# Optimization experiments

Measured on AMD Instinct MI355X. Metric: run time of the kernel, lower is better.

## Reference

```python
import jax, jax.numpy as jnp
import numpy as np
from jax import lax

B, C, H, W = 16, 128, 64, 64
AUX = 2 * 128 + 20 + 1  # hybrid: edge(128)+seg(128)+pred_edge(1)+pred_seg(20)
PATCHES = [(2, 2), (4, 4)]


def conv1x1(x, w, b):
    # w: [O, I]
    return jnp.einsum('bchw,oc->bohw', x, w) + b[None, :, None, None]


def conv3x3(x, w, b, pad, dil=1):
    y = lax.conv_general_dilated(x, w, (1, 1), [(pad, pad), (pad, pad)],
                                 rhs_dilation=(dil, dil),
                                 dimension_numbers=('NCHW', 'OIHW', 'NCHW'))
    return y + b[None, :, None, None]


def layernorm_chw(x, eps=1e-5):
    # LayerNorm over [C,H,W] per sample, no affine
    mu = x.mean(axis=(1, 2, 3), keepdims=True)
    var = ((x - mu) ** 2).mean(axis=(1, 2, 3), keepdims=True)
    return (x - mu) / jnp.sqrt(var + eps)


def adn(x, aux, ew, eb, sw, sb, bw, bb):
    a = conv1x1(aux, ew, eb)
    gamma = conv1x1(a, sw, sb)
    beta = conv1x1(jnp.concatenate([x, a], axis=1), bw, bb)
    return layernorm_chw(x) * gamma + beta


def window_attn(q, k, v, ph, pw):
    b, dk, h, w = q.shape
    oh, ow = h // ph, w // pw

    def patch(t):  # [b,dk,h,w] -> [b, oh*ow, dk*ph*pw]
        t = t.reshape(b, dk, oh, ph, ow, pw)
        return t.transpose(0, 2, 4, 1, 3, 5).reshape(b, oh * ow, dk * ph * pw)

    Q, K, V = patch(q), patch(k), patch(v)
    scale = 1.0 / jnp.sqrt(jnp.asarray(Q.shape[-1], Q.dtype))
    scores = jnp.einsum('bnd,bmd->bnm', Q, K) * scale
    y = jnp.einsum('bnm,bmd->bnd', jax.nn.softmax(scores, axis=-1), V)
    y = y.reshape(b, oh, ow, dk, ph, pw).transpose(0, 3, 1, 4, 2, 5).reshape(b, dk, h, w)
    return y


def mssa_forward(p):
    (x, edge, seg, pred_edge, pred_seg,
     q_w, q_b, k_w, k_b, v_w, v_b,
     d1_embed_w, d1_embed_b, d1_scale_w, d1_scale_b, d1_bias_w, d1_bias_b,
     d2_embed_w, d2_embed_b, d2_scale_w, d2_scale_b, d2_bias_w, d2_bias_b,
     sc_w, sc_b, bi1_w, bi1_b, bi2_w, bi2_b) = p

    aux = jnp.concatenate([edge, seg, pred_edge, pred_seg], axis=1)

    q = adn(conv1x1(x, q_w, q_b), aux, d1_embed_w, d1_embed_b, d1_scale_w, d1_scale_b, d1_bias_w, d1_bias_b)
    k = adn(conv1x1(x, k_w, k_b), aux, d1_embed_w, d1_embed_b, d1_scale_w, d1_scale_b, d1_bias_w, d1_bias_b)
    v = adn(conv1x1(x, v_w, v_b), aux, d1_embed_w, d1_embed_b, d1_scale_w, d1_scale_b, d1_bias_w, d1_bias_b)

    qs = jnp.split(q, len(PATCHES), axis=1)
    ks = jnp.split(k, len(PATCHES), axis=1)
    vs = jnp.split(v, len(PATCHES), axis=1)
    outs = [window_attn(qs[i], ks[i], vs[i], PATCHES[i][1], PATCHES[i][0]) for i in range(len(PATCHES))]

    mid = x + jnp.concatenate(outs, axis=1)
    o = adn(mid, aux, d2_embed_w, d2_embed_b, d2_scale_w, d2_scale_b, d2_bias_w, d2_bias_b)
    gamma = jnp.tanh(conv3x3(o, sc_w, sc_b, pad=1))
    beta = conv3x3(jax.nn.gelu(conv3x3(o, bi1_w, bi1_b, pad=2, dil=2), approximate=False), bi2_w, bi2_b, pad=1)
    return mid * gamma + beta


def setup_inputs() -> dict:
    key = jax.random.key(0)
    ks = iter(jax.random.split(key, 40))
    nrm = lambda shape, s=1.0: jax.random.normal(next(ks), shape, jnp.float32) * s
    P = 0.02  # param init scale
    inp = {
        'x': nrm((B, C, H, W)),
        'edge': nrm((B, 128, H, W)),
        'seg': nrm((B, 128, H, W)),
        'pred_edge': jax.random.uniform(next(ks), (B, 1, H, W), jnp.float32),
        'pred_seg': jax.random.uniform(next(ks), (B, 20, H, W), jnp.float32),
        'q_w': nrm((C, C), P), 'q_b': jnp.zeros((C,), jnp.float32),
        'k_w': nrm((C, C), P), 'k_b': jnp.zeros((C,), jnp.float32),
        'v_w': nrm((C, C), P), 'v_b': jnp.zeros((C,), jnp.float32),
        'd1_embed_w': nrm((C, AUX), P), 'd1_embed_b': jnp.zeros((C,), jnp.float32),
        'd1_scale_w': nrm((C, C), P), 'd1_scale_b': jnp.ones((C,), jnp.float32),
        'd1_bias_w': nrm((C, 2 * C), P), 'd1_bias_b': jnp.zeros((C,), jnp.float32),
        'd2_embed_w': nrm((C, AUX), P), 'd2_embed_b': jnp.zeros((C,), jnp.float32),
        'd2_scale_w': nrm((C, C), P), 'd2_scale_b': jnp.ones((C,), jnp.float32),
        'd2_bias_w': nrm((C, 2 * C), P), 'd2_bias_b': jnp.zeros((C,), jnp.float32),
        'sc_w': nrm((C, C, 3, 3), P), 'sc_b': jnp.zeros((C,), jnp.float32),
        'bi1_w': nrm((C, C, 3, 3), P), 'bi1_b': jnp.zeros((C,), jnp.float32),
        'bi2_w': nrm((C, C, 3, 3), P), 'bi2_b': jnp.zeros((C,), jnp.float32),
    }
    return inp


def reference(x, edge, seg, pred_edge, pred_seg,
              q_w, q_b, k_w, k_b, v_w, v_b,
              d1_embed_w, d1_embed_b, d1_scale_w, d1_scale_b, d1_bias_w, d1_bias_b,
              d2_embed_w, d2_embed_b, d2_scale_w, d2_scale_b, d2_bias_w, d2_bias_b,
              sc_w, sc_b, bi1_w, bi1_b, bi2_w, bi2_b):
    return mssa_forward((x, edge, seg, pred_edge, pred_seg,
                         q_w, q_b, k_w, k_b, v_w, v_b,
                         d1_embed_w, d1_embed_b, d1_scale_w, d1_scale_b, d1_bias_w, d1_bias_b,
                         d2_embed_w, d2_embed_b, d2_scale_w, d2_scale_b, d2_bias_w, d2_bias_b,
                         sc_w, sc_b, bi1_w, bi1_b, bi2_w, bi2_b))
```

## Files before the change

### kernel.cpp

```cpp
#include <hip/hip_runtime.h>
#include <cstdint>

typedef unsigned short ushort_t;
typedef unsigned int uint_t;
typedef __attribute__((ext_vector_type(8))) short short8;
typedef __attribute__((ext_vector_type(4))) float f32x4;

#define MFMA16(a, b, c) __builtin_amdgcn_mfma_f32_16x16x32_bf16((a), (b), (c), 0, 0, 0)
#define SWZ(c, r) ((((c) + ((r) >> 2)) & 3))
#define INV_N 1.9073486328125e-6f

struct P4 { ushort_t* p[4]; };
struct B4 { const float* b[4]; };

__device__ __forceinline__ ushort_t f2bf(float f) {
    uint_t u = __builtin_bit_cast(uint_t, f);
    u += 0x7FFFu + ((u >> 16) & 1u);
    return (ushort_t)(u >> 16);
}
__device__ __forceinline__ float bf2f(ushort_t h) {
    return __builtin_bit_cast(float, (uint_t)h << 16);
}

__global__ __launch_bounds__(256) void prep_w(
    ushort_t* wb, const float* qw, const float* kw, const float* vw,
    const float* ew1, const float* ew2, const float* sw1, const float* sw2,
    const float* bw1, const float* bw2,
    const float* scw, const float* b1w, const float* b2w)
{
    int idx = blockIdx.x * 256 + threadIdx.x;
    if (idx >= 663552) return;
    float v;
    if (idx < 49152) {
        int z = idx >> 14, r = idx & 16383;
        v = (z == 0 ? qw : z == 1 ? kw : vw)[r];
    } else if (idx < 122880) {
        int j = idx - 49152; int z = j / 36864; int jj = j - z * 36864;
        int o = jj / 288, k = jj - o * 288;
        v = (k < 277) ? (z ? ew2 : ew1)[o * 277 + k] : 0.f;
    } else if (idx < 155648) {
        int j = idx - 122880; int z = j >> 14;
        v = (z ? sw2 : sw1)[j & 16383];
    } else if (idx < 221184) {
        int j = idx - 155648; int z = j >> 15;
        v = (z ? bw2 : bw1)[j & 32767];
    } else {
        int j = idx - 221184;
        const float* src = j < 147456 ? scw : j < 294912 ? b1w : b2w;
        j = j % 147456;
        int tap = j >> 14, r = (j >> 7) & 127, c = j & 127;
        v = src[r * 1152 + c * 9 + tap];
    }
    wb[idx] = f2bf(v);
}

__global__ __launch_bounds__(256) void combine_w(ushort_t* wc, const ushort_t* wb)
{
    __shared__ float ews[128 * 33];
    __shared__ ushort_t Ws[128 * 130];
    int z = blockIdx.y, nt = blockIdx.x, n0 = nt * 32;
    int t = threadIdx.x;
    const ushort_t* wew = wb + 49152;
    const ushort_t* wsw = wb + 122880;
    const ushort_t* wbw = wb + 155648;
    const ushort_t* W; int wstr, wof;
    if (z == 0)      { W = wsw;         wstr = 128; wof = 0; }
    else if (z == 1) { W = wbw;         wstr = 256; wof = 128; }
    else if (z == 2) { W = wsw + 16384; wstr = 128; wof = 0; }
    else             { W = wbw + 32768; wstr = 256; wof = 128; }
    const ushort_t* E = wew + (z >= 2 ? 36864 : 0);
    for (int s = t; s < 16384; s += 256) {
        int c = s & 127, o = s >> 7;
        Ws[c * 130 + o] = W[o * wstr + wof + c];
    }
    for (int s = t; s < 4096; s += 256) {
        int c = s >> 5, n = s & 31;
        ews[c * 33 + n] = bf2f(E[c * 288 + n0 + n]);
    }
    __syncthreads();
    int o = t & 127, nh = t >> 7;
    float acc[16];
#pragma unroll
    for (int i = 0; i < 16; ++i) acc[i] = 0.f;
    for (int c = 0; c < 128; ++c) {
        float wv = bf2f(Ws[c * 130 + o]);
#pragma unroll
        for (int i = 0; i < 16; ++i) acc[i] += wv * ews[c * 33 + nh * 16 + i];
    }
#pragma unroll
    for (int i = 0; i < 16; ++i)
        wc[(size_t)(z * 128 + o) * 288 + n0 + nh * 16 + i] = f2bf(acc[i]);
}

__global__ __launch_bounds__(512) void combine_bias(
    float* bc, const float* sw1, const float* bw1, const float* sw2, const float* bw2,
    const float* eb1, const float* eb2, const float* sb1, const float* bb1,
    const float* sb2, const float* bb2)
{
    int t = threadIdx.x; int z = t >> 7, o = t & 127;
    const float* W; int wstr, wof; const float* eb; float add;
    if (z == 0)      { W = sw1; wstr = 128; wof = 0;   eb = eb1; add = sb1[o]; }
    else if (z == 1) { W = bw1; wstr = 256; wof = 128; eb = eb1; add = bb1[o]; }
    else if (z == 2) { W = sw2; wstr = 128; wof = 0;   eb = eb2; add = sb2[o]; }
    else             { W = bw2; wstr = 256; wof = 128; eb = eb2; add = bb2[o]; }
    float s = add;
    for (int c = 0; c < 128; ++c) s += W[o * wstr + wof + c] * eb[c];
    bc[t] = s;
}

__global__ __launch_bounds__(256) void transp_x(const float* __restrict__ x, ushort_t* __restrict__ xT)
{
    __shared__ ushort_t tile[64 * 130];
    int b = blockIdx.y, p0 = blockIdx.x * 64;
    int t = threadIdx.x;
#pragma unroll
    for (int i = 0; i < 8; ++i) {
        int s = t + i * 256;
        int c = s >> 4, p4 = (s & 15) * 4;
        float4 f = *(const float4*)(x + ((size_t)(b * 128 + c) << 12) + p0 + p4);
        tile[(p4 + 0) * 130 + c] = f2bf(f.x);
        tile[(p4 + 1) * 130 + c] = f2bf(f.y);
        tile[(p4 + 2) * 130 + c] = f2bf(f.z);
        tile[(p4 + 3) * 130 + c] = f2bf(f.w);
    }
    __syncthreads();
#pragma unroll
    for (int i = 0; i < 4; ++i) {
        int s = t + i * 256;
        int p = s >> 4, c8 = (s & 15) * 8;
        ushort_t v[8];
#pragma unroll
        for (int e = 0; e < 8; ++e) v[e] = tile[p * 130 + c8 + e];
        uint4 ov = {(uint_t)v[0] | ((uint_t)v[1] << 16), (uint_t)v[2] | ((uint_t)v[3] << 16),
                    (uint_t)v[4] | ((uint_t)v[5] << 16), (uint_t)v[6] | ((uint_t)v[7] << 16)};
        *(uint4*)(xT + ((size_t)(b * 4096) + p0 + p) * 128 + c8) = ov;
    }
}

__global__ __launch_bounds__(256) void transp_aux(const float* __restrict__ edge, const float* __restrict__ seg,
                                                  const float* __restrict__ pe, const float* __restrict__ ps,
                                                  ushort_t* __restrict__ auxT)
{
    __shared__ ushort_t tile[64 * 292];
    int b = blockIdx.y, p0 = blockIdx.x * 64;
    int t = threadIdx.x;
#pragma unroll
    for (int i = 0; i < 18; ++i) {
        int s = t + i * 256;
        int c = s >> 4, p4 = (s & 15) * 4;
        float4 f = {0.f, 0.f, 0.f, 0.f};
        if (c < 128)       f = *(const float4*)(edge + ((size_t)(b * 128 + c) << 12) + p0 + p4);
        else if (c < 256)  f = *(const float4*)(seg + ((size_t)(b * 128 + c - 128) << 12) + p0 + p4);
        else if (c == 256) f = *(const float4*)(pe + ((size_t)b << 12) + p0 + p4);
        else if (c < 277)  f = *(const float4*)(ps + ((size_t)(b * 20 + c - 257) << 12) + p0 + p4);
        tile[(p4 + 0) * 292 + c] = f2bf(f.x);
        tile[(p4 + 1) * 292 + c] = f2bf(f.y);
        tile[(p4 + 2) * 292 + c] = f2bf(f.z);
        tile[(p4 + 3) * 292 + c] = f2bf(f.w);
    }
    __syncthreads();
#pragma unroll
    for (int i = 0; i < 9; ++i) {
        int s = t + i * 256;
        int p = s / 36, c8 = (s % 36) * 8;
        ushort_t v[8];
#pragma unroll
        for (int e = 0; e < 8; ++e) v[e] = tile[p * 292 + c8 + e];
        uint4 ov = {(uint_t)v[0] | ((uint_t)v[1] << 16), (uint_t)v[2] | ((uint_t)v[3] << 16),
                    (uint_t)v[4] | ((uint_t)v[5] << 16), (uint_t)v[6] | ((uint_t)v[7] << 16)};
        *(uint4*)(auxT + ((size_t)(b * 4096) + p0 + p) * 288 + c8) = ov;
    }
}

template <int EP>
__global__ __launch_bounds__(256) void gemm_conv(
    const ushort_t* bA, int Kb1, size_t zBoff,
    const ushort_t* wA, int wstride, int wAperZ, int NK,
    B4 bias4, P4 out4, const ushort_t* gT, const ushort_t* betT,
    float* stats, int dostats)
{
    constexpr int LDSZ = (EP == 2) ? 33792 : 34816;
    __shared__ char lds[LDSZ];
    int b = blockIdx.y, bx = blockIdx.x, z = blockIdx.z;
    int t = threadIdx.x, lane = t & 63, w = t >> 6;
    int wm = w & 1, wn = w >> 1, lo = lane & 15, quad = lane >> 4;
    const ushort_t* wAz = wA + (wAperZ ? (size_t)z * 128 * wstride : 0);
    const ushort_t* bAz = bA + (size_t)z * zBoff;
    ushort_t* outp = out4.p[z];
    size_t bbase = (size_t)b * 4096;
    int y0 = 0, x0 = 0;
    if (EP == 2) { y0 = (bx >> 1) * 4; x0 = (bx & 1) * 32; }

    f32x4 acc[4][4];
#pragma unroll
    for (int i = 0; i < 4; ++i)
#pragma unroll
        for (int j = 0; j < 4; ++j) acc[i][j] = (f32x4){0.f, 0.f, 0.f, 0.f};

    int r0 = t >> 2, c0 = t & 3, r1 = r0 + 64;
    int gp0, gp1;
    if (EP == 2) {
        gp0 = (y0 + (r0 >> 5)) * 64 + x0 + (r0 & 31);
        gp1 = (y0 + (r1 >> 5)) * 64 + x0 + (r1 & 31);
    } else {
        gp0 = bx * 128 + r0;
        gp1 = bx * 128 + r1;
    }
    const ushort_t* bRow0 = bAz + (bbase + gp0) * Kb1;
    const ushort_t* bRow1 = bAz + (bbase + gp1) * Kb1;
    uint4 pfA0 = *(const uint4*)(wAz + (size_t)r0 * wstride + c0 * 8);
    uint4 pfA1 = *(const uint4*)(wAz + (size_t)r1 * wstride + c0 * 8);
    uint4 pfB0 = *(const uint4*)(bRow0 + c0 * 8);
    uint4 pfB1 = *(const uint4*)(bRow1 + c0 * 8);
    for (int ck = 0; ck < NK; ++ck) {
        __syncthreads();
        *(uint4*)(lds + r0 * 64 + SWZ(c0, r0) * 16) = pfA0;
        *(uint4*)(lds + r1 * 64 + SWZ(c0, r1) * 16) = pfA1;
        *(uint4*)(lds + 8192 + r0 * 64 + SWZ(c0, r0) * 16) = pfB0;
        *(uint4*)(lds + 8192 + r1 * 64 + SWZ(c0, r1) * 16) = pfB1;
        __syncthreads();
        if (ck + 1 < NK) {
            int k0 = (ck + 1) * 32;
            pfA0 = *(const uint4*)(wAz + (size_t)r0 * wstride + k0 + c0 * 8);
            pfA1 = *(const uint4*)(wAz + (size_t)r1 * wstride + k0 + c0 * 8);
            pfB0 = *(const uint4*)(bRow0 + k0 + c0 * 8);
            pfB1 = *(const uint4*)(bRow1 + k0 + c0 * 8);
        }
        short8 af[4];
#pragma unroll
        for (int mt = 0; mt < 4; ++mt) {
            int row = wm * 64 + mt * 16 + lo;
            af[mt] = *(const short8*)(lds + row * 64 + SWZ(quad, row) * 16);
        }
#pragma unroll
        for (int nt = 0; nt < 4; ++nt) {
            int n = wn * 64 + nt * 16 + lo;
            short8 bf = *(const short8*)(lds + 8192 + n * 64 + SWZ(quad, n) * 16);
#pragma unroll
            for (int mt = 0; mt < 4; ++mt) acc[mt][nt] = MFMA16(af[mt], bf, acc[mt][nt]);
        }
    }

    float mean = 0.f, rstd = 0.f;
    if (EP >= 2) {
        int slot = (EP == 3) ? 3 : z;
        float s0 = stats[(slot * 16 + b) * 2], s1 = stats[(slot * 16 + b) * 2 + 1];
        mean = s0 * INV_N;
        rstd = rsqrtf(fmaxf(s1 * INV_N - mean * mean, 0.f) + 1e-5f);
    }
    float lsum = 0.f, lss = 0.f;
    if (EP == 2) {
        __syncthreads();
        ushort_t* Cs = (ushort_t*)lds;
#pragma unroll
        for (int mt = 0; mt < 4; ++mt)
#pragma unroll
            for (int nt = 0; nt < 4; ++nt) {
                int oo0 = wm * 64 + mt * 16 + quad * 4;
                int pp = wn * 64 + nt * 16 + lo;
                int gp = (y0 + (pp >> 5)) * 64 + x0 + (pp & 31);
                size_t tbase = (bbase + gp) * 128 + oo0;
                ushort4 tv = *(const ushort4*)(bAz + tbase);
                ushort4 gv = *(const ushort4*)(gT + tbase);
                ushort4 bv = *(const ushort4*)(betT + tbase);
#pragma unroll
                for (int r = 0; r < 4; ++r) {
                    float v = acc[mt][nt][r] + bf2f((&bv.x)[r])
                            + (bf2f((&tv.x)[r]) - mean) * rstd * bf2f((&gv.x)[r]);
                    Cs[(oo0 + r) * 132 + pp] = f2bf(v);
                }
            }
        __syncthreads();
        if (z < 2) {
            for (int s = t; s < 1024; s += 256) {
                int n_l = s >> 5, fq = s & 31;
                int ypair = n_l >> 4, xp = n_l & 15;
                ushort_t tmp[8];
#pragma unroll
                for (int e = 0; e < 8; ++e) {
                    int f = fq * 8 + e;
                    int c = f >> 2, py = (f >> 1) & 1, px = f & 1;
                    tmp[e] = Cs[c * 132 + (ypair * 2 + py) * 32 + xp * 2 + px];
                }
                int n = ((y0 >> 1) + ypair) * 32 + (x0 >> 1) + xp;
                uint4 ov = {(uint_t)tmp[0] | ((uint_t)tmp[1] << 16), (uint_t)tmp[2] | ((uint_t)tmp[3] << 16),
                            (uint_t)tmp[4] | ((uint_t)tmp[5] << 16), (uint_t)tmp[6] | ((uint_t)tmp[7] << 16)};
                *(uint4*)(outp + ((size_t)(b * 1024 + n) << 8) + fq * 8) = ov;
            }
            for (int s = t; s < 1024; s += 256) {
                int n_l = s >> 7, fq = s & 127;
                ushort_t tmp[8];
#pragma unroll
                for (int e = 0; e < 8; ++e) {
                    int f = fq * 8 + e;
                    int c = f >> 4, py = (f >> 2) & 3, px = f & 3;
                    tmp[e] = Cs[(64 + c) * 132 + py * 32 + n_l * 4 + px];
                }
                int n = (y0 >> 2) * 16 + (x0 >> 2) + n_l;
                uint4 ov = {(uint_t)tmp[0] | ((uint_t)tmp[1] << 16), (uint_t)tmp[2] | ((uint_t)tmp[3] << 16),
                            (uint_t)tmp[4] | ((uint_t)tmp[5] << 16), (uint_t)tmp[6] | ((uint_t)tmp[7] << 16)};
                *(uint4*)(outp + 4194304u + ((size_t)(b * 256 + n) << 10) + fq * 8) = ov;
            }
        } else {
            for (int s = t; s < 2048; s += 256) {
                int f = s >> 3, j = s & 7;
                int ypair = j >> 2, xq = j & 3;
                int c = f >> 2, py = (f >> 1) & 1, px = f & 1;
                ushort_t tmp[4];
#pragma unroll
                for (int i2 = 0; i2 < 4; ++i2)
                    tmp[i2] = Cs[c * 132 + (ypair * 2 + py) * 32 + (xq * 4 + i2) * 2 + px];
                int m0 = ((y0 >> 1) + ypair) * 32 + (x0 >> 1) + xq * 4;
                uint2 ov = {(uint_t)tmp[0] | ((uint_t)tmp[1] << 16), (uint_t)tmp[2] | ((uint_t)tmp[3] << 16)};
                *(uint2*)(outp + ((size_t)(b * 256 + f) << 10) + m0) = ov;
            }
            for (int s = t; s < 2048; s += 256) {
                int f = s >> 1, j = s & 1;
                int c = f >> 4, py = (f >> 2) & 3, px = f & 3;
                ushort_t tmp[4];
#pragma unroll
                for (int i2 = 0; i2 < 4; ++i2)
                    tmp[i2] = Cs[(64 + c) * 132 + py * 32 + (j * 4 + i2) * 4 + px];
                int m0 = (y0 >> 2) * 16 + (x0 >> 2) + j * 4;
                uint2 ov = {(uint_t)tmp[0] | ((uint_t)tmp[1] << 16), (uint_t)tmp[2] | ((uint_t)tmp[3] << 16)};
                *(uint2*)(outp + 4194304u + ((size_t)(b * 1024 + f) << 8) + m0) = ov;
            }
        }
    } else {
        ushort_t* Cs = (ushort_t*)lds;
        __syncthreads();
#pragma unroll
        for (int mt = 0; mt < 4; ++mt)
#pragma unroll
            for (int nt = 0; nt < 4; ++nt) {
                int oo0 = wm * 64 + mt * 16 + quad * 4;
                int pp = wn * 64 + nt * 16 + lo;
                float vv[4];
                if (EP == 0) {
#pragma unroll
                    for (int r = 0; r < 4; ++r) vv[r] = acc[mt][nt][r] + bias4.b[z][oo0 + r];
                    if (dostats) {
#pragma unroll
                        for (int r = 0; r < 4; ++r) { lsum += vv[r]; lss += vv[r] * vv[r]; }
                    }
                } else {
                    size_t tbase = (bbase + bx * 128 + pp) * 128 + oo0;
                    ushort4 tv = *(const ushort4*)(bAz + tbase);
                    ushort4 gv = *(const ushort4*)(gT + tbase);
                    ushort4 bv = *(const ushort4*)(betT + tbase);
#pragma unroll
                    for (int r = 0; r < 4; ++r)
                        vv[r] = acc[mt][nt][r] + bf2f((&bv.x)[r])
                              + (bf2f((&tv.x)[r]) - mean) * rstd * bf2f((&gv.x)[r]);
                }
                ushort4 st = {f2bf(vv[0]), f2bf(vv[1]), f2bf(vv[2]), f2bf(vv[3])};
                *(ushort4*)(&Cs[pp * 136 + oo0]) = st;
            }
        __syncthreads();
        if (EP == 3) {
#pragma unroll
            for (int i = 0; i < 2; ++i) {
                int c = t + i * 256;
                int cc2 = c >> 7, pp = c & 127;
                size_t dst = ((size_t)(b * 4 + cc2) * 4096 + bx * 128 + pp) * 32;
#pragma unroll
                for (int j = 0; j < 4; ++j)
                    *(uint4*)(outp + dst + j * 8) = *(const uint4*)(&Cs[pp * 136 + cc2 * 32 + j * 8]);
            }
        } else {
            int pp = t >> 1, hf = t & 1;
            size_t gofs = (bbase + bx * 128 + pp) * 128 + hf * 64;
#pragma unroll
            for (int i = 0; i < 8; ++i)
                *(uint4*)(outp + gofs + i * 8) = *(const uint4*)(&Cs[pp * 136 + hf * 64 + i * 8]);
        }
    }
    if (EP == 0 && dostats) {
#pragma unroll
        for (int o2 = 32; o2 >= 1; o2 >>= 1) { lsum += __shfl_xor(lsum, o2); lss += __shfl_xor(lss, o2); }
        __syncthreads();
        float* red = (float*)lds;
        if (lane == 0) { red[w * 2] = lsum; red[w * 2 + 1] = lss; }
        __syncthreads();
        if (t == 0) {
            atomicAdd(&stats[(z * 16 + b) * 2], red[0] + red[2] + red[4] + red[6]);
            atomicAdd(&stats[(z * 16 + b) * 2 + 1], red[1] + red[3] + red[5] + red[7]);
        }
    }
}

template <int EP>
__global__ __launch_bounds__(256) void gemm_attn(
    const ushort_t* A, size_t aBS, const ushort_t* Bm, size_t bBS,
    int Ka, int NK, float scale,
    ushort_t* sout, size_t soBS, int soNb,
    const ushort_t* xT, ushort_t* midT, float* stats)
{
    constexpr int LDSZ = (EP >= 1) ? 33792 : 34816;
    __shared__ char lds[LDSZ];
    int b = blockIdx.z, my = blockIdx.y, nx = blockIdx.x;
    int t = threadIdx.x, lane = t & 63, w = t >> 6;
    int wm = w & 1, wn = w >> 1, lo = lane & 15, quad = lane >> 4;

    f32x4 acc[4][4];
#pragma unroll
    for (int i = 0; i < 4; ++i)
#pragma unroll
        for (int j = 0; j < 4; ++j) acc[i][j] = (f32x4){0.f, 0.f, 0.f, 0.f};

    const ushort_t* Ab = A + b * aBS + (size_t)(my * 128) * Ka;
    const ushort_t* Bb = Bm + b * bBS + (size_t)(nx * 128) * Ka;
    int r0 = t >> 2, c0 = t & 3, r1 = r0 + 64;
    uint4 pfA0 = *(const uint4*)(Ab + (size_t)r0 * Ka + c0 * 8);
    uint4 pfA1 = *(const uint4*)(Ab + (size_t)r1 * Ka + c0 * 8);
    uint4 pfB0 = *(const uint4*)(Bb + (size_t)r0 * Ka + c0 * 8);
    uint4 pfB1 = *(const uint4*)(Bb + (size_t)r1 * Ka + c0 * 8);
    for (int ck = 0; ck < NK; ++ck) {
        __syncthreads();
        *(uint4*)(lds + r0 * 64 + SWZ(c0, r0) * 16) = pfA0;
        *(uint4*)(lds + r1 * 64 + SWZ(c0, r1) * 16) = pfA1;
        *(uint4*)(lds + 8192 + r0 * 64 + SWZ(c0, r0) * 16) = pfB0;
        *(uint4*)(lds + 8192 + r1 * 64 + SWZ(c0, r1) * 16) = pfB1;
        __syncthreads();
        if (ck + 1 < NK) {
            int k0 = (ck + 1) * 32;
            pfA0 = *(const uint4*)(Ab + (size_t)r0 * Ka + k0 + c0 * 8);
            pfA1 = *(const uint4*)(Ab + (size_t)r1 * Ka + k0 + c0 * 8);
            pfB0 = *(const uint4*)(Bb + (size_t)r0 * Ka + k0 + c0 * 8);
            pfB1 = *(const uint4*)(Bb + (size_t)r1 * Ka + k0 + c0 * 8);
        }
        short8 af[4];
#pragma unroll
        for (int mt = 0; mt < 4; ++mt) {
            int row = wm * 64 + mt * 16 + lo;
            af[mt] = *(const short8*)(lds + row * 64 + SWZ(quad, row) * 16);
        }
#pragma unroll
        for (int nt = 0; nt < 4; ++nt) {
            int n = wn * 64 + nt * 16 + lo;
            short8 bf = *(const short8*)(lds + 8192 + n * 64 + SWZ(quad, n) * 16);
#pragma unroll
            for (int mt = 0; mt < 4; ++mt) acc[mt][nt] = MFMA16(af[mt], bf, acc[mt][nt]);
        }
    }

    if (EP == 0) {
        ushort_t* Cs = (ushort_t*)lds;
        __syncthreads();
#pragma unroll
        for (int mt = 0; mt < 4; ++mt)
#pragma unroll
            for (int nt = 0; nt < 4; ++nt) {
                int rr0 = wm * 64 + mt * 16 + quad * 4;
                int cl = wn * 64 + nt * 16 + lo;
                ushort4 st = {f2bf(acc[mt][nt][0] * scale), f2bf(acc[mt][nt][1] * scale),
                              f2bf(acc[mt][nt][2] * scale), f2bf(acc[mt][nt][3] * scale)};
                *(ushort4*)(&Cs[cl * 136 + rr0]) = st;
            }
        __syncthreads();
        {
            int rr = t >> 1, hf = t & 1;
            size_t gbase = (size_t)b * soBS + (size_t)(my * 128 + rr) * soNb + nx * 128 + hf * 64;
#pragma unroll
            for (int i = 0; i < 8; ++i) {
                ushort_t e[8];
#pragma unroll
                for (int j = 0; j < 8; ++j) e[j] = Cs[(hf * 64 + i * 8 + j) * 136 + rr];
                uint4 ov = {(uint_t)e[0] | ((uint_t)e[1] << 16), (uint_t)e[2] | ((uint_t)e[3] << 16),
                            (uint_t)e[4] | ((uint_t)e[5] << 16), (uint_t)e[6] | ((uint_t)e[7] << 16)};
                *(uint4*)(sout + gbase + i * 8) = ov;
            }
        }
        return;
    }
    __syncthreads();
    ushort_t* Cs = (ushort_t*)lds;
#pragma unroll
    for (int mt = 0; mt < 4; ++mt)
#pragma unroll
        for (int nt = 0; nt < 4; ++nt)
#pragma unroll
            for (int reg = 0; reg < 4; ++reg) {
                int r_l = wm * 64 + mt * 16 + quad * 4 + reg;
                int c_l = wn * 64 + nt * 16 + lo;
                Cs[r_l * 132 + c_l] = f2bf(acc[mt][nt][reg]);
            }
    __syncthreads();
    float lsum = 0.f, lss = 0.f;
    for (int s = t; s < 4096; s += 256) {
        int sp, r_l, cbase, pybit, pxbit;
        if (EP == 1) {
            int sp_l = s >> 3, cj = s & 7;
            int y_l = sp_l >> 6, xv = sp_l & 63;
            r_l = (y_l >> 1) * 32 + (xv >> 1);
            sp = (my * 8 + y_l) * 64 + xv;
            cbase = nx * 32 + cj * 4;
            pybit = (y_l & 1) * 2 + (xv & 1);
            pxbit = 4;
        } else {
            int sp_l = s >> 1, cj = s & 1;
            int y_l = sp_l >> 6, xv = sp_l & 63;
            r_l = (y_l >> 2) * 16 + (xv >> 2);
            sp = (my * 32 + y_l) * 64 + xv;
            cbase = 64 + nx * 8 + cj * 4;
            pybit = (y_l & 3) * 4 + (xv & 3);
            pxbit = 16;
        }
        size_t base = ((size_t)(b * 4096) + sp) * 128 + cbase;
        ushort4 xv4 = *(const ushort4*)(xT + base);
        int c_l0 = (EP == 1) ? (cbase - nx * 32) * 4 + pybit : (cbase - 64 - nx * 8) * 16 + pybit;
        ushort_t o4[4];
#pragma unroll
        for (int ci = 0; ci < 4; ++ci) {
            float vm = bf2f(Cs[r_l * 132 + c_l0 + ci * pxbit]) + bf2f((&xv4.x)[ci]);
            o4[ci] = f2bf(vm);
            lsum += vm; lss += vm * vm;
        }
        ushort4 st = {o4[0], o4[1], o4[2], o4[3]};
        *(ushort4*)(midT + base) = st;
    }
#pragma unroll
    for (int o2 = 32; o2 >= 1; o2 >>= 1) { lsum += __shfl_xor(lsum, o2); lss += __shfl_xor(lss, o2); }
    __syncthreads();
    float* red = (float*)lds;
    if (lane == 0) { red[w * 2] = lsum; red[w * 2 + 1] = lss; }
    __syncthreads();
    if (t == 0) {
        atomicAdd(&stats[(3 * 16 + b) * 2], red[0] + red[2] + red[4] + red[6]);
        atomicAdd(&stats[(3 * 16 + b) * 2 + 1], red[1] + red[3] + red[5] + red[7]);
    }
}

__global__ __launch_bounds__(256) void softmax_k(ushort_t* SP)
{
    int wid = blockIdx.x * 4 + (threadIdx.x >> 6);
    int lane = threadIdx.x & 63;
    ushort_t* row;
    int PL;
    if (wid < 16384) { row = SP + ((size_t)wid << 10); PL = 16; }
    else { int r2 = wid - 16384; row = SP + 16777216u + ((size_t)r2 << 8); PL = 4; }
    float v[16];
    float mx = -1e30f;
    for (int i = 0; i < PL; ++i) { v[i] = bf2f(row[lane + (i << 6)]); mx = fmaxf(mx, v[i]); }
#pragma unroll
    for (int o = 32; o >= 1; o >>= 1) mx = fmaxf(mx, __shfl_xor(mx, o));
    float sum = 0.f;
    for (int i = 0; i < PL; ++i) { v[i] = __expf(v[i] - mx); sum += v[i]; }
#pragma unroll
    for (int o = 32; o >= 1; o >>= 1) sum += __shfl_xor(sum, o);
    float inv = 1.f / sum;
    for (int i = 0; i < PL; ++i) row[lane + (i << 6)] = f2bf(v[i] * inv);
}

__global__ __launch_bounds__(1024) void conv3x3_dual(
    const ushort_t* __restrict__ inT, const ushort_t* __restrict__ wtA, const ushort_t* __restrict__ wtB,
    const float* __restrict__ biasA, const float* __restrict__ biasB,
    ushort_t* __restrict__ outA, ushort_t* __restrict__ outB)
{
    __shared__ char lds[73728 + 12 * 68 * 64];
    char* Braw = lds + 73728;
    int b = blockIdx.y, z = blockIdx.z;
    int dil = 1 + z;
    int NRr = 8 + 2 * dil;
    const ushort_t* wt = z ? wtB : wtA;
    const float* bias = z ? biasB : biasA;
    ushort_t* out = z ? outB : outA;
    int y0 = blockIdx.x * 8;
    int t = threadIdx.x, lane = t & 63, w = t >> 6;
    int wm = w & 1, wr = w >> 1, lo = lane & 15, quad = lane >> 4;

    f32x4 acc[4][4];
#pragma unroll
    for (int i = 0; i < 4; ++i)
#pragma unroll
        for (int j = 0; j < 4; ++j) acc[i][j] = (f32x4){0.f, 0.f, 0.f, 0.f};

    for (int cc = 0; cc < 4; ++cc) {
        if (cc) __syncthreads();
        for (int s = t; s < 4608; s += 1024) {
            int tap = s >> 9, r = (s >> 2) & 127, c = s & 3;
            uint4 v = *(const uint4*)(wt + ((size_t)(tap * 128 + r) << 7) + cc * 32 + c * 8);
            *(uint4*)(lds + tap * 8192 + r * 64 + SWZ(c, r) * 16) = v;
        }
        int NSLOT = NRr * 272;
        for (int s = t; s < NSLOT; s += 1024) {
            int c4 = s & 3;
            int pr = s >> 2;
            int xx = pr % 68, rr = pr / 68;
            int ys = y0 - dil + rr;
            int ix = xx - dil;
            uint4 v = {0u, 0u, 0u, 0u};
            if (ys >= 0 && ys < 64 && (unsigned)ix < 64u)
                v = *(const uint4*)(inT + ((size_t)((b * 4 + cc) * 4096 + ys * 64 + ix)) * 32 + c4 * 8);
            *(uint4*)(Braw + pr * 64 + SWZ(c4, pr) * 16) = v;
        }
        __syncthreads();
#pragma unroll
        for (int tap = 0; tap < 9; ++tap) {
            int ky = tap / 3, kx = tap % 3;
            short8 af[4];
#pragma unroll
            for (int mt = 0; mt < 4; ++mt) {
                int row = wm * 64 + mt * 16 + lo;
                af[mt] = *(const short8*)(lds + tap * 8192 + row * 64 + SWZ(quad, row) * 16);
            }
#pragma unroll
            for (int nt = 0; nt < 4; ++nt) {
                int pr = (wr + ky * dil) * 68 + nt * 16 + lo + kx * dil;
                short8 bf = *(const short8*)(Braw + pr * 64 + SWZ(quad, pr) * 16);
#pragma unroll
                for (int mt = 0; mt < 4; ++mt) acc[mt][nt] = MFMA16(af[mt], bf, acc[mt][nt]);
            }
        }
    }
    for (int h = 0; h < 2; ++h) {
        __syncthreads();
        if ((wr >> 2) == h) {
            int rl = wr & 3;
#pragma unroll
            for (int mt = 0; mt < 4; ++mt)
#pragma unroll
                for (int nt = 0; nt < 4; ++nt) {
                    int oo0 = wm * 64 + mt * 16 + quad * 4;
                    int col = nt * 16 + lo;
                    ushort4 st;
#pragma unroll
                    for (int r = 0; r < 4; ++r) {
                        float v = acc[mt][nt][r] + bias[oo0 + r];
                        if (z == 0) v = tanhf(v);
                        else        v = 0.5f * v * (1.f + erff(v * 0.70710678118654752f));
                        (&st.x)[r] = f2bf(v);
                    }
                    int byo = ((rl * 64 + col) * 256 + oo0 * 2) ^ ((col & 15) << 4);
                    *(ushort4*)(lds + byo) = st;
                }
        }
        __syncthreads();
        if (z == 0) {
            int rl2 = t >> 8, col2 = (t >> 2) & 63, k2 = t & 3;
            char* dst = (char*)out + (((size_t)(b * 4096) + (y0 + h * 4 + rl2) * 64 + col2) << 8) + k2 * 64;
            int bb = (rl2 * 64 + col2) * 256 + k2 * 64;
            int sw = (col2 & 15) << 4;
#pragma unroll
            for (int i = 0; i < 4; ++i)
                *(uint4*)(dst + i * 16) = *(const uint4*)(lds + ((bb + i * 16) ^ sw));
        } else {
            int cc2 = t >> 8, s_l = t & 255;
            int rl2 = s_l >> 6, col2 = s_l & 63;
            ushort_t* dst = out + ((size_t)((b * 4 + cc2) * 4096) + (y0 + h * 4 + rl2) * 64 + col2) * 32;
            int bb = (rl2 * 64 + col2) * 256 + cc2 * 64;
            int sw = (col2 & 15) << 4;
#pragma unroll
            for (int i = 0; i < 4; ++i)
                *(uint4*)(dst + i * 8) = *(const uint4*)(lds + ((bb + i * 16) ^ sw));
        }
    }
}

__global__ __launch_bounds__(512) void conv3x3_final(
    const ushort_t* __restrict__ inT, const ushort_t* __restrict__ wt, const float* __restrict__ bias,
    float* __restrict__ out, const ushort_t* __restrict__ midT, const ushort_t* __restrict__ g3T)
{
    __shared__ char lds[73728 + 6 * 68 * 64];
    char* Braw = lds + 73728;
    int b = blockIdx.y;
    int y0 = blockIdx.x * 4;
    int t = threadIdx.x, lane = t & 63, w = t >> 6;
    int wm = w & 1, wr = w >> 1, lo = lane & 15, quad = lane >> 4;

    f32x4 acc[4][4];
#pragma unroll
    for (int i = 0; i < 4; ++i)
#pragma unroll
        for (int j = 0; j < 4; ++j) acc[i][j] = (f32x4){0.f, 0.f, 0.f, 0.f};

    for (int cc = 0; cc < 4; ++cc) {
        if (cc) __syncthreads();
        for (int s = t; s < 4608; s += 512) {
            int tap = s >> 9, r = (s >> 2) & 127, c = s & 3;
            uint4 v = *(const uint4*)(wt + ((size_t)(tap * 128 + r) << 7) + cc * 32 + c * 8);
            *(uint4*)(lds + tap * 8192 + r * 64 + SWZ(c, r) * 16) = v;
        }
        for (int s = t; s < 1632; s += 512) {
            int c4 = s & 3;
            int pr = s >> 2;
            int xx = pr % 68, rr = pr / 68;
            int ys = y0 - 1 + rr;
            int ix = xx - 1;
            uint4 v = {0u, 0u, 0u, 0u};
            if (ys >= 0 && ys < 64 && (unsigned)ix < 64u)
                v = *(const uint4*)(inT + ((size_t)((b * 4 + cc) * 4096 + ys * 64 + ix)) * 32 + c4 * 8);
            *(uint4*)(Braw + pr * 64 + SWZ(c4, pr) * 16) = v;
        }
        __syncthreads();
#pragma unroll
        for (int tap = 0; tap < 9; ++tap) {
            int ky = tap / 3, kx = tap % 3;
            short8 af[4];
#pragma unroll
            for (int mt = 0; mt < 4; ++mt) {
                int row = wm * 64 + mt * 16 + lo;
                af[mt] = *(const short8*)(lds + tap * 8192 + row * 64 + SWZ(quad, row) * 16);
            }
#pragma unroll
            for (int nt = 0; nt < 4; ++nt) {
                int pr = (wr + ky) * 68 + nt * 16 + lo + kx;
                short8 bf = *(const short8*)(Braw + pr * 64 + SWZ(quad, pr) * 16);
#pragma unroll
                for (int mt = 0; mt < 4; ++mt) acc[mt][nt] = MFMA16(af[mt], bf, acc[mt][nt]);
            }
        }
    }
#pragma unroll
    for (int mt = 0; mt < 4; ++mt)
#pragma unroll
        for (int nt = 0; nt < 4; ++nt) {
            int oo0 = wm * 64 + mt * 16 + quad * 4;
            int col = nt * 16 + lo;
            int sp = (y0 + wr) * 64 + col;
            size_t tbase = ((size_t)(b * 4096) + sp) * 128 + oo0;
            ushort4 mv = *(const ushort4*)(midT + tbase);
            ushort4 gv = *(const ushort4*)(g3T + tbase);
#pragma unroll
            for (int r = 0; r < 4; ++r) {
                int oo = oo0 + r;
                size_t off = ((size_t)(b * 128 + oo) << 12) + sp;
                out[off] = bf2f((&mv.x)[r]) * bf2f((&gv.x)[r]) + acc[mt][nt][r] + bias[oo];
            }
        }
}

extern "C" void kernel_launch(void* const* d_in, const int* in_sizes, int n_in,
                              void* d_out, int out_size, void* d_ws, size_t ws_size,
                              hipStream_t stream)
{
    const float* x    = (const float*)d_in[0];
    const float* edge = (const float*)d_in[1];
    const float* seg  = (const float*)d_in[2];
    const float* pe   = (const float*)d_in[3];
    const float* ps   = (const float*)d_in[4];
    const float* q_w  = (const float*)d_in[5];  const float* q_b  = (const float*)d_in[6];
    const float* k_w  = (const float*)d_in[7];  const float* k_b  = (const float*)d_in[8];
    const float* v_w  = (const float*)d_in[9];  const float* v_b  = (const float*)d_in[10];
    const float* d1_ew = (const float*)d_in[11]; const float* d1_eb = (const float*)d_in[12];
    const float* d1_sw = (const float*)d_in[13]; const float* d1_sb = (const float*)d_in[14];
    const float* d1_bw = (const float*)d_in[15]; const float* d1_bb = (const float*)d_in[16];
    const float* d2_ew = (const float*)d_in[17]; const float* d2_eb = (const float*)d_in[18];
    const float* d2_sw = (const float*)d_in[19]; const float* d2_sb = (const float*)d_in[20];
    const float* d2_bw = (const float*)d_in[21]; const float* d2_bb = (const float*)d_in[22];
    const float* sc_w  = (const float*)d_in[23]; const float* sc_b  = (const float*)d_in[24];
    const float* bi1_w = (const float*)d_in[25]; const float* bi1_b = (const float*)d_in[26];
    const float* bi2_w = (const float*)d_in[27]; const float* bi2_b = (const float*)d_in[28];

    char* ws = (char*)d_ws;
    ushort_t* wb = (ushort_t*)ws;
    ushort_t* wc = (ushort_t*)(ws + 1327360);
    float* bc    = (float*)(ws + 1622272);
    float* stats = (float*)(ws + 1624320);
    char* RA = ws + 1703936;
    char* RB = RA + 37748736;
    char* RC = RB + 16777216;
    char* RD = RC + 50331648;
    char* RE = RD + 16777216;
    char* RF = RE + 16777216;
    char* RG = RF + 16777216;
    char* RH = RG + 16777216;
    char* RI = RH + 33554432;

    ushort_t* auxT = (ushort_t*)RA;
    ushort_t* SP0  = (ushort_t*)RA;
    ushort_t* xT   = (ushort_t*)RB;
    ushort_t* q0T  = (ushort_t*)RC;
    ushort_t* midT = (ushort_t*)RC;
    ushort_t* oT   = (ushort_t*)(RC + 16777216);
    ushort_t* g1   = (ushort_t*)RD;
    ushort_t* g3   = (ushort_t*)RD;
    ushort_t* betA1= (ushort_t*)RE;
    ushort_t* g2   = (ushort_t*)RF;
    ushort_t* betA2= (ushort_t*)RG;
    ushort_t* Qp   = (ushort_t*)RH;
    ushort_t* Kp   = Qp + 8388608;
    ushort_t* VT   = (ushort_t*)RI;
    ushort_t* tT   = (ushort_t*)RI;
    const size_t ZB = 8388608;

    dim3 blk(256);

    hipMemsetAsync(stats, 0, 512, stream);
    prep_w<<<2592, blk, 0, stream>>>(wb, q_w, k_w, v_w, d1_ew, d2_ew, d1_sw, d2_sw, d1_bw, d2_bw, sc_w, bi1_w, bi2_w);
    combine_bias<<<1, 512, 0, stream>>>(bc, d1_sw, d1_bw, d2_sw, d2_bw, d1_eb, d2_eb, d1_sb, d1_bb, d2_sb, d2_bb);
    combine_w<<<dim3(9, 4), blk, 0, stream>>>(wc, wb);
    transp_x<<<dim3(64, 16), blk, 0, stream>>>(x, xT);
    transp_aux<<<dim3(64, 16), blk, 0, stream>>>(edge, seg, pe, ps, auxT);

    gemm_conv<0><<<dim3(32, 16, 4), blk, 0, stream>>>(auxT, 288, 0, wc, 288, 1, 9,
        B4{{bc, bc + 128, bc + 256, bc + 384}}, P4{{g1, betA1, g2, betA2}}, nullptr, nullptr, stats, 0);
    gemm_conv<0><<<dim3(32, 16, 3), blk, 0, stream>>>(xT, 128, 0, wb, 128, 1, 4,
        B4{{q_b, k_b, v_b, nullptr}}, P4{{q0T, q0T + ZB, q0T + 2 * ZB, nullptr}}, nullptr, nullptr, stats, 1);
    gemm_conv<2><<<dim3(32, 16, 3), blk, 0, stream>>>(q0T, 128, ZB, wb + 155648, 256, 0, 4,
        B4{{nullptr, nullptr, nullptr, nullptr}}, P4{{Qp, Kp, VT, nullptr}}, g1, betA1, stats, 0);

    gemm_attn<0><<<dim3(8, 8, 16), blk, 0, stream>>>(Qp, 262144, Kp, 262144, 256, 8, 0.0625f,
        SP0, 1048576, 1024, nullptr, nullptr, stats);
    gemm_attn<0><<<dim3(2, 2, 16), blk, 0, stream>>>(Qp + 4194304, 262144, Kp + 4194304, 262144, 1024, 32, 0.03125f,
        SP0 + 16777216, 65536, 256, nullptr, nullptr, stats);
    softmax_k<<<5120, blk, 0, stream>>>(SP0);
    gemm_attn<1><<<dim3(2, 8, 16), blk, 0, stream>>>(SP0, 1048576, VT, 262144, 1024, 32, 1.f,
        nullptr, 0, 0, xT, midT, stats);
    gemm_attn<2><<<dim3(8, 2, 16), blk, 0, stream>>>(SP0 + 16777216, 65536, VT + 4194304, 262144, 256, 8, 1.f,
        nullptr, 0, 0, xT, midT, stats);

    gemm_conv<3><<<dim3(32, 16, 1), blk, 0, stream>>>(midT, 128, 0, wb + 155648 + 32768, 256, 0, 4,
        B4{{nullptr, nullptr, nullptr, nullptr}}, P4{{oT, nullptr, nullptr, nullptr}}, g2, betA2, stats, 0);

    conv3x3_dual<<<dim3(8, 16, 2), dim3(1024), 0, stream>>>(oT, wb + 221184, wb + 368640, sc_b, bi1_b, g3, tT);
    conv3x3_final<<<dim3(16, 16), dim3(512), 0, stream>>>(tT, wb + 516096, bi2_b, (float*)d_out, midT, g3);
}
```

Measured before the change: 649.4 us.

## Stack multiple output-weight slabs per block to reuse activation tiles

Measured after the change: 735.1 us. +13.2%, slower.

```diff
diff --git a/kernel.cpp b/kernel.cpp
--- a/kernel.cpp
+++ b/kernel.cpp
@@ -172,6 +172,117 @@
     }
 }
 
+template <int NS, int DOSTATS>
+__global__ __launch_bounds__(NS * 256) void gemm_stack(
+    const ushort_t* __restrict__ bA, int K, const ushort_t* __restrict__ Wstk, int NK,
+    B4 bias4, P4 out4, float* stats)
+{
+    constexpr int STAGE = NS * 8192 + 8192;
+    constexpr int LDSZ = (STAGE > 34816) ? STAGE : 34816;
+    __shared__ char lds[LDSZ];
+    int b = blockIdx.y, bx = blockIdx.x;
+    int t = threadIdx.x, lane = t & 63, w = t >> 6;
+    int wm = w >> 1, wn = w & 1, lo = lane & 15, quad = lane >> 4;
+    size_t bbase = (size_t)b * 4096;
+
+    f32x4 acc[4][4];
+#pragma unroll
+    for (int i = 0; i < 4; ++i)
+#pragma unroll
+        for (int j = 0; j < 4; ++j) acc[i][j] = (f32x4){0.f, 0.f, 0.f, 0.f};
+
+    const int TOT = (NS + 1) * 512;
+    uint4 pf[3];
+#pragma unroll
+    for (int i = 0; i < 3; ++i) {
+        int s = t + i * NS * 256;
+        if (s < TOT) {
+            if (s < NS * 512) { int q = s >> 2, c = s & 3; pf[i] = *(const uint4*)(Wstk + (size_t)q * K + c * 8); }
+            else { int r = (s - NS * 512) >> 2, c = s & 3; pf[i] = *(const uint4*)(bA + (bbase + bx * 128 + r) * (size_t)K + c * 8); }
+        }
+    }
+    for (int ck = 0; ck < NK; ++ck) {
+        __syncthreads();
+#pragma unroll
+        for (int i = 0; i < 3; ++i) {
+            int s = t + i * NS * 256;
+            if (s < TOT) {
+                int off;
+                if (s < NS * 512) { int q = s >> 2, c = s & 3; off = q * 64 + SWZ(c, q) * 16; }
+                else { int r = (s - NS * 512) >> 2, c = s & 3; off = NS * 8192 + r * 64 + SWZ(c, r) * 16; }
+                *(uint4*)(lds + off) = pf[i];
+            }
+        }
+        __syncthreads();
+        if (ck + 1 < NK) {
+            int k0 = (ck + 1) * 32;
+#pragma unroll
+            for (int i = 0; i < 3; ++i) {
+                int s = t + i * NS * 256;
+                if (s < TOT) {
+                    if (s < NS * 512) { int q = s >> 2, c = s & 3; pf[i] = *(const uint4*)(Wstk + (size_t)q * K + k0 + c * 8); }
+                    else { int r = (s - NS * 512) >> 2, c = s & 3; pf[i] = *(const uint4*)(bA + (bbase + bx * 128 + r) * (size_t)K + k0 + c * 8); }
+                }
+            }
+        }
+        short8 af[4];
+#pragma unroll
+        for (int mt = 0; mt < 4; ++mt) {
+            int row = wm * 64 + mt * 16 + lo;
+            af[mt] = *(const short8*)(lds + row * 64 + SWZ(quad, row) * 16);
+        }
+#pragma unroll
+        for (int nt = 0; nt < 4; ++nt) {
+            int n = wn * 64 + nt * 16 + lo;
+            short8 bf = *(const short8*)(lds + NS * 8192 + n * 64 + SWZ(quad, n) * 16);
+#pragma unroll
+            for (int mt = 0; mt < 4; ++mt) acc[mt][nt] = MFMA16(af[mt], bf, acc[mt][nt]);
+        }
+    }
+
+    ushort_t* Cs = (ushort_t*)lds;
+    for (int z = 0; z < NS; ++z) {
+        __syncthreads();
+        if ((wm >> 1) == z) {
+            float lsum = 0.f, lss = 0.f;
+#pragma unroll
+            for (int mt = 0; mt < 4; ++mt)
+#pragma unroll
+                for (int nt = 0; nt < 4; ++nt) {
+                    int oo0 = (wm & 1) * 64 + mt * 16 + quad * 4;
+                    int pp = wn * 64 + nt * 16 + lo;
+                    float vv[4];
+#pragma unroll
+                    for (int r = 0; r < 4; ++r) vv[r] = acc[mt][nt][r] + bias4.b[z][oo0 + r];
+                    if (DOSTATS) {
+#pragma unroll
+                        for (int r = 0; r < 4; ++r) { lsum += vv[r]; lss += vv[r] * vv[r]; }
+                    }
+                    ushort4 st = {f2bf(vv[0]), f2bf(vv[1]), f2bf(vv[2]), f2bf(vv[3])};
+                    *(ushort4*)(&Cs[pp * 136 + oo0]) = st;
+                }
+            if (DOSTATS) {
+#pragma unroll
+                for (int o2 = 32; o2 >= 1; o2 >>= 1) { lsum += __shfl_xor(lsum, o2); lss += __shfl_xor(lss, o2); }
+                if (lane == 0) {
+                    atomicAdd(&stats[(z * 16 + b) * 2], lsum);
+                    atomicAdd(&stats[(z * 16 + b) * 2 + 1], lss);
+                }
+            }
+        }
+        __syncthreads();
+        ushort_t* outp = out4.p[z];
+#pragma unroll
+        for (int i = 0; i < 3; ++i) {
+            int c3 = t + i * NS * 256;
+            if (c3 < 2048) {
+                int pp = c3 >> 4, ii = c3 & 15;
+                *(uint4*)(outp + (bbase + bx * 128 + pp) * 128 + ii * 8) = *(const uint4*)(&Cs[pp * 136 + ii * 8]);
+            }
+        }
+    }
+}
+
 template <int EP>
 __global__ __launch_bounds__(256) void gemm_conv(
     const ushort_t* bA, int Kb1, size_t zBoff,
@@ -242,13 +353,12 @@
     }
 
     float mean = 0.f, rstd = 0.f;
-    if (EP >= 2) {
+    {
         int slot = (EP == 3) ? 3 : z;
         float s0 = stats[(slot * 16 + b) * 2], s1 = stats[(slot * 16 + b) * 2 + 1];
         mean = s0 * INV_N;
         rstd = rsqrtf(fmaxf(s1 * INV_N - mean * mean, 0.f) + 1e-5f);
     }
-    float lsum = 0.f, lss = 0.f;
     if (EP == 2) {
         __syncthreads();
         ushort_t* Cs = (ushort_t*)lds;
@@ -336,55 +446,26 @@
                 int oo0 = wm * 64 + mt * 16 + quad * 4;
                 int pp = wn * 64 + nt * 16 + lo;
                 float vv[4];
-                if (EP == 0) {
-#pragma unroll
-                    for (int r = 0; r < 4; ++r) vv[r] = acc[mt][nt][r] + bias4.b[z][oo0 + r];
-                    if (dostats) {
-#pragma unroll
-                        for (int r = 0; r < 4; ++r) { lsum += vv[r]; lss += vv[r] * vv[r]; }
-                    }
-                } else {
-                    size_t tbase = (bbase + bx * 128 + pp) * 128 + oo0;
-                    ushort4 tv = *(const ushort4*)(bAz + tbase);
-                    ushort4 gv = *(const ushort4*)(gT + tbase);
-                    ushort4 bv = *(const ushort4*)(betT + tbase);
-#pragma unroll
-                    for (int r = 0; r < 4; ++r)
-                        vv[r] = acc[mt][nt][r] + bf2f((&bv.x)[r])
-                              + (bf2f((&tv.x)[r]) - mean) * rstd * bf2f((&gv.x)[r]);
-                }
+                size_t tbase = (bbase + bx * 128 + pp) * 128 + oo0;
+                ushort4 tv = *(const ushort4*)(bAz + tbase);
+                ushort4 gv = *(const ushort4*)(gT + tbase);
+                ushort4 bv = *(const ushort4*)(betT + tbase);
+#pragma unroll
+                for (int r = 0; r < 4; ++r)
+                    vv[r] = acc[mt][nt][r] + bf2f((&bv.x)[r])
+                          + (bf2f((&tv.x)[r]) - mean) * rstd * bf2f((&gv.x)[r]);
                 ushort4 st = {f2bf(vv[0]), f2bf(vv[1]), f2bf(vv[2]), f2bf(vv[3])};
                 *(ushort4*)(&Cs[pp * 136 + oo0]) = st;
             }
         __syncthreads();
-        if (EP == 3) {
-#pragma unroll
-            for (int i = 0; i < 2; ++i) {
-                int c = t + i * 256;
-                int cc2 = c >> 7, pp = c & 127;
-                size_t dst = ((size_t)(b * 4 + cc2) * 4096 + bx * 128 + pp) * 32;
-#pragma unroll
-                for (int j = 0; j < 4; ++j)
-                    *(uint4*)(outp + dst + j * 8) = *(const uint4*)(&Cs[pp * 136 + cc2 * 32 + j * 8]);
-            }
-        } else {
-            int pp = t >> 1, hf = t & 1;
-            size_t gofs = (bbase + bx * 128 + pp) * 128 + hf * 64;
-#pragma unroll
-            for (int i = 0; i < 8; ++i)
-                *(uint4*)(outp + gofs + i * 8) = *(const uint4*)(&Cs[pp * 136 + hf * 64 + i * 8]);
-        }
-    }
-    if (EP == 0 && dostats) {
-#pragma unroll
-        for (int o2 = 32; o2 >= 1; o2 >>= 1) { lsum += __shfl_xor(lsum, o2); lss += __shfl_xor(lss, o2); }
-        __syncthreads();
-        float* red = (float*)lds;
-        if (lane == 0) { red[w * 2] = lsum; red[w * 2 + 1] = lss; }
-        __syncthreads();
-        if (t == 0) {
-            atomicAdd(&stats[(z * 16 + b) * 2], red[0] + red[2] + red[4] + red[6]);
-            atomicAdd(&stats[(z * 16 + b) * 2 + 1], red[1] + red[3] + red[5] + red[7]);
+#pragma unroll
+        for (int i = 0; i < 2; ++i) {
+            int c = t + i * 256;
+            int cc2 = c >> 7, pp = c & 127;
+            size_t dst = ((size_t)(b * 4 + cc2) * 4096 + bx * 128 + pp) * 32;
+#pragma unroll
+            for (int j = 0; j < 4; ++j)
+                *(uint4*)(outp + dst + j * 8) = *(const uint4*)(&Cs[pp * 136 + cc2 * 32 + j * 8]);
         }
     }
 }
@@ -678,7 +759,7 @@
         if (cc) __syncthreads();
         for (int s = t; s < 4608; s += 512) {
             int tap = s >> 9, r = (s >> 2) & 127, c = s & 3;
-            uint4 v = *(const uint4*)(wt + ((size_t)(tap * 128 + r) << 7) + cc * 32 + c * 8);
+            uint4 v = *(const uint4*)(wt + ((size_t)((tap)*128 + r) << 7) + cc * 32 + c * 8);
             *(uint4*)(lds + tap * 8192 + r * 64 + SWZ(c, r) * 16) = v;
         }
         for (int s = t; s < 1632; s += 512) {
@@ -793,10 +874,10 @@
     transp_x<<<dim3(64, 16), blk, 0, stream>>>(x, xT);
     transp_aux<<<dim3(64, 16), blk, 0, stream>>>(edge, seg, pe, ps, auxT);
 
-    gemm_conv<0><<<dim3(32, 16, 4), blk, 0, stream>>>(auxT, 288, 0, wc, 288, 1, 9,
-        B4{{bc, bc + 128, bc + 256, bc + 384}}, P4{{g1, betA1, g2, betA2}}, nullptr, nullptr, stats, 0);
-    gemm_conv<0><<<dim3(32, 16, 3), blk, 0, stream>>>(xT, 128, 0, wb, 128, 1, 4,
-        B4{{q_b, k_b, v_b, nullptr}}, P4{{q0T, q0T + ZB, q0T + 2 * ZB, nullptr}}, nullptr, nullptr, stats, 1);
+    gemm_stack<4, 0><<<dim3(32, 16), dim3(1024), 0, stream>>>(auxT, 288, wc, 9,
+        B4{{bc, bc + 128, bc + 256, bc + 384}}, P4{{g1, betA1, g2, betA2}}, stats);
+    gemm_stack<3, 1><<<dim3(32, 16), dim3(768), 0, stream>>>(xT, 128, wb, 4,
+        B4{{q_b, k_b, v_b, nullptr}}, P4{{q0T, q0T + ZB, q0T + 2 * ZB, nullptr}}, stats);
     gemm_conv<2><<<dim3(32, 16, 3), blk, 0, stream>>>(q0T, 128, ZB, wb + 155648, 256, 0, 4,
         B4{{nullptr, nullptr, nullptr, nullptr}}, P4{{Qp, Kp, VT, nullptr}}, g1, betA1, stats, 0);
 
```
